# Performance work log

Hardware: AMD Instinct MI355X
Metric: run time of the kernel (lower is better)

## Reference

```python
import jax, jax.numpy as jnp
import numpy as np

EPS = 1e-5

def batchnorm1d(x, g, b):
    # train-mode batch stats over (B, N); x: (B, C, N)
    m = x.mean(axis=(0, 2), keepdims=True)
    v = x.var(axis=(0, 2), keepdims=True)
    return (x - m) * jax.lax.rsqrt(v + EPS) * g[None, :, None] + b[None, :, None]

def instancenorm2d(x, g, b):
    # x: (B, Q, S, K), normalize per-sample per-channel over (S, K)
    m = x.mean(axis=(2, 3), keepdims=True)
    v = x.var(axis=(2, 3), keepdims=True)
    return (x - m) * jax.lax.rsqrt(v + EPS) * g[None, :, None, None] + b[None, :, None, None]

def gather_nbrs(t, idx):
    # t: (B, C, N), idx: (B, S, K) -> (B, C, S, K)
    return jnp.take_along_axis(t[:, :, :, None], idx[:, None, :, :], axis=2)

def pw_conv(x, w, b):
    # 1x1 Conv1d: x (B,C,N), w (O,C), b (O,)
    return jnp.einsum('oc,bcn->bon', w, x) + b[None, :, None]

def fkaconv(x, pos, sup, idx, fc1_w, fc2_w, fc3_w, in1_g, in1_b, in2_g, in2_b,
            alpha, beta, norm_radius, cv_w):
    pts = gather_nbrs(pos, idx) - sup[:, :, :, None]            # (B,3,S,K) local coords
    feat = gather_nbrs(x, idx)                                  # (B,C,S,K)
    # distances computed on detached pts (as in torch)
    d = jnp.sqrt((jax.lax.stop_gradient(pts) ** 2).sum(axis=1))  # (B,S,K)
    dw = jax.nn.sigmoid(-alpha * d + beta)                       # (B,S,K)
    s = dw.sum(axis=2, keepdims=True)
    s = s + (s == 0).astype(dw.dtype) + 1e-6
    dw = (dw / s * d.shape[2])[:, None]                          # (B,1,S,K)
    p = pts / norm_radius
    mat = jax.nn.relu(instancenorm2d(jnp.einsum('qd,bdsk->bqsk', fc1_w, p), in1_g, in1_b))
    mp = jnp.broadcast_to((mat * dw).max(axis=3, keepdims=True), mat.shape)
    mat = jnp.concatenate([mat, mp], axis=1)
    mat = jax.nn.relu(instancenorm2d(jnp.einsum('qc,bcsk->bqsk', fc2_w, mat), in2_g, in2_b))
    mp = jnp.broadcast_to((mat * dw).max(axis=3, keepdims=True), mat.shape)
    mat = jnp.concatenate([mat, mp], axis=1)
    mat = jax.nn.relu(jnp.einsum('qc,bcsk->bqsk', fc3_w, mat)) * dw  # (B,Q,S,K)
    agg = jnp.einsum('bcsk,bqsk->bcsq', feat, mat)               # (B,C,S,Q)
    return jnp.einsum('bcsq,ocq->bos', agg, cv_w)                # (B,O,S)

def setup_inputs() -> dict:
    key = jax.random.key(0)
    ks = iter(jax.random.split(key, 40))
    B, Cin, Cmid, Cout, N, S, K, Q = 16, 128, 64, 256, 8192, 2048, 16, 16
    f = lambda *sh: jax.random.normal(next(ks), sh, dtype=jnp.float32) * 0.05
    inp = {
        'x': jax.random.normal(next(ks), (B, Cin, N), dtype=jnp.float32),
        'pos': jax.random.normal(next(ks), (B, 3, N), dtype=jnp.float32),
        'support_points': jax.random.normal(next(ks), (B, 3, S), dtype=jnp.float32),
        'neighbors_indices': jax.random.randint(next(ks), (B, S, K), 0, N),
        'mask_indices': jnp.ones((B, S, K), dtype=jnp.int32),
        # cv0 + bn0
        'cv0_w': f(Cmid, Cin), 'cv0_b': f(Cmid),
        'bn0_g': jnp.ones((Cmid,), jnp.float32), 'bn0_b': jnp.zeros((Cmid,), jnp.float32),
        # FKAConv params
        'fc1_w': f(Q, 3), 'fc2_w': f(Q, 2 * Q), 'fc3_w': f(Q, 2 * Q),
        'in1_g': jnp.ones((Q,), jnp.float32), 'in1_b': jnp.zeros((Q,), jnp.float32),
        'in2_g': jnp.ones((Q,), jnp.float32), 'in2_b': jnp.zeros((Q,), jnp.float32),
        'alpha': jnp.ones((1,), jnp.float32), 'beta': jnp.ones((1,), jnp.float32),
        'norm_radius': jnp.ones((1,), jnp.float32),
        'cv_w': f(Cmid, Cmid, Q),
        'bn1_g': jnp.ones((Cmid,), jnp.float32), 'bn1_b': jnp.zeros((Cmid,), jnp.float32),
        # cv2 + bn2
        'cv2_w': f(Cout, Cmid), 'cv2_b': f(Cout),
        'bn2_g': jnp.ones((Cout,), jnp.float32), 'bn2_b': jnp.zeros((Cout,), jnp.float32),
        # shortcut
        'sc_w': f(Cout, Cin), 'sc_b': f(Cout),
        'bnsc_g': jnp.ones((Cout,), jnp.float32), 'bnsc_b': jnp.zeros((Cout,), jnp.float32),
    }
    return inp

def reference(x, pos, support_points, neighbors_indices, mask_indices,
              cv0_w, cv0_b, bn0_g, bn0_b,
              fc1_w, fc2_w, fc3_w, in1_g, in1_b, in2_g, in2_b,
              alpha, beta, norm_radius, cv_w, bn1_g, bn1_b,
              cv2_w, cv2_b, bn2_g, bn2_b, sc_w, sc_b, bnsc_g, bnsc_b):
    # sampling() / radius_nn() are passthroughs when precomputed (POCO usage)
    idx = neighbors_indices
    h = jax.nn.relu(batchnorm1d(pw_conv(x, cv0_w, cv0_b), bn0_g, bn0_b))          # (B,64,N)
    h = fkaconv(h, pos, support_points, idx, fc1_w, fc2_w, fc3_w,
                in1_g, in1_b, in2_g, in2_b, alpha, beta, norm_radius, cv_w)       # (B,64,S)
    h = jax.nn.relu(batchnorm1d(h, bn1_g, bn1_b))
    h = batchnorm1d(pw_conv(h, cv2_w, cv2_b), bn2_g, bn2_b)                        # (B,256,S)
    sc = batchnorm1d(pw_conv(x, sc_w, sc_b), bnsc_g, bnsc_b)                       # (B,256,N)
    sc = gather_nbrs(sc, idx).max(axis=3)                                          # max_pool -> (B,256,S)
    return jax.nn.relu(h + sc)

if __name__ == '__main__':
    out = reference(**setup_inputs())
    print(out.shape)
```

## Files before the change

### kernel.cpp

```cpp
#include <hip/hip_runtime.h>
#include <hip/hip_bf16.h>

#define DEV static __device__ __forceinline__

typedef __attribute__((ext_vector_type(8))) short bf16x8;
typedef __attribute__((ext_vector_type(4))) float f32x4;

#define ST_SC_BN0  0
#define ST_SH_BN0  64
#define ST_SC_SC   128
#define ST_SH_SC   384
#define ST_SC_IN1  640
#define ST_SH_IN1  896
#define ST_SC_IN2  1152
#define ST_SH_IN2  1408
#define ST_SC_BN1  1664
#define ST_SH_BN1  1728
#define ST_SC_BN2  1792
#define ST_SH_BN2  2048

DEV float rsum16(float v){
#pragma unroll
  for (int off = 8; off >= 1; off >>= 1) v += __shfl_xor(v, off, 16);
  return v;
}
DEV float rmax16(float v){
#pragma unroll
  for (int off = 8; off >= 1; off >>= 1) v = fmaxf(v, __shfl_xor(v, off, 16));
  return v;
}

__global__ __launch_bounds__(256) void k_prep_w(
    const float* __restrict__ cv0w, const float* __restrict__ scw,
    const float* __restrict__ cvw,  const float* __restrict__ cv2w,
    __hip_bfloat16* __restrict__ wb, __hip_bfloat16* __restrict__ cvb,
    __hip_bfloat16* __restrict__ cv2b)
{
  int i = blockIdx.x * 256 + threadIdx.x;
  if (i < 40960){
    float v = (i < 8192) ? cv0w[i] : scw[i - 8192];
    wb[i] = __float2bfloat16(v);
  } else if (i < 106496){
    cvb[i - 40960] = __float2bfloat16(cvw[i - 40960]);
  } else {
    cv2b[i - 106496] = __float2bfloat16(cv2w[i - 106496]);
  }
}

__global__ __launch_bounds__(256) void k_xpose(
    const float* __restrict__ x, __hip_bfloat16* __restrict__ xb)
{
  __shared__ float t[128][65];
  const int tid = threadIdx.x;
  const int b = blockIdx.x >> 7, nt = blockIdx.x & 127;
  const int n0 = nt << 6;
#pragma unroll
  for (int p = 0; p < 8; p++){
    int row = (p << 4) + (tid >> 4);
    float4 v = *(const float4*)&x[(((size_t)b * 128 + row) << 13) + n0 + ((tid & 15) << 2)];
    t[row][(tid & 15) * 4 + 0] = v.x;
    t[row][(tid & 15) * 4 + 1] = v.y;
    t[row][(tid & 15) * 4 + 2] = v.z;
    t[row][(tid & 15) * 4 + 3] = v.w;
  }
  __syncthreads();
  const int k8 = tid & 15;
#pragma unroll
  for (int p = 0; p < 4; p++){
    int n = (p << 4) + (tid >> 4);
    union { uint4 u; __hip_bfloat16 e[8]; } pk;
#pragma unroll
    for (int j = 0; j < 8; j++) pk.e[j] = __float2bfloat16(t[k8 * 8 + j][n]);
    *(uint4*)&xb[((size_t)(b << 13) + n0 + n) * 128 + k8 * 8] = pk.u;
  }
}

__global__ __launch_bounds__(256) void k1_mfma(
    const __hip_bfloat16* __restrict__ xb, const __hip_bfloat16* __restrict__ wb,
    const float* __restrict__ cv0b, const float* __restrict__ scb,
    __hip_bfloat16* __restrict__ y0t, __hip_bfloat16* __restrict__ sct,
    float* __restrict__ p1)
{
  const int tid = threadIdx.x;
  const int b = blockIdx.x >> 7, nt = blockIdx.x & 127;
  const int n0 = nt << 6;
  const int wv = tid >> 6, l = tid & 63;
  const int lr = l & 15, lg = l >> 4;
  float* p1row = p1 + (size_t)blockIdx.x * 640;

  f32x4 acc[5][4];
#pragma unroll
  for (int i = 0; i < 5; i++)
#pragma unroll
    for (int j = 0; j < 4; j++) acc[i][j] = (f32x4){0.f, 0.f, 0.f, 0.f};

  const __hip_bfloat16* xrow = xb + ((size_t)(b << 13) + n0 + lr) * 128 + lg * 8;
  const __hip_bfloat16* wrow = wb + (size_t)(wv * 80 + lr) * 128 + lg * 8;

#pragma unroll
  for (int ks = 0; ks < 4; ks++){
    bf16x8 B[4], A[5];
#pragma unroll
    for (int nf = 0; nf < 4; nf++) B[nf] = *(const bf16x8*)(xrow + nf * 2048 + ks * 32);
#pragma unroll
    for (int mf = 0; mf < 5; mf++) A[mf] = *(const bf16x8*)(wrow + mf * 2048 + ks * 32);
#pragma unroll
    for (int mf = 0; mf < 5; mf++)
#pragma unroll
      for (int nf = 0; nf < 4; nf++)
        acc[mf][nf] = __builtin_amdgcn_mfma_f32_16x16x32_bf16(A[mf], B[nf], acc[mf][nf], 0, 0, 0);
  }

#pragma unroll
  for (int mf = 0; mf < 5; mf++){
    const int m0 = wv * 80 + mf * 16 + lg * 4;
    float bv[4];
#pragma unroll
    for (int r = 0; r < 4; r++){
      int m = m0 + r;
      bv[r] = (m < 64) ? cv0b[m] : scb[m - 64];
    }
#pragma unroll
    for (int nf = 0; nf < 4; nf++)
#pragma unroll
      for (int r = 0; r < 4; r++) acc[mf][nf][r] += bv[r];

#pragma unroll
    for (int nf = 0; nf < 4; nf++){
      int n = n0 + nf * 16 + lr;
      union { uint2 u; __hip_bfloat16 e[4]; } pk;
#pragma unroll
      for (int r = 0; r < 4; r++) pk.e[r] = __float2bfloat16(acc[mf][nf][r]);
      if (m0 < 64)
        *(uint2*)&y0t[((size_t)(b << 13) + n) * 64 + m0] = pk.u;
      else
        *(uint2*)&sct[((size_t)(b << 13) + n) * 256 + (m0 - 64)] = pk.u;
    }
#pragma unroll
    for (int r = 0; r < 4; r++){
      float ss = 0.f, qq = 0.f;
#pragma unroll
      for (int nf = 0; nf < 4; nf++){ float v = acc[mf][nf][r]; ss += v; qq += v * v; }
#pragma unroll
      for (int off = 8; off >= 1; off >>= 1){
        ss += __shfl_xor(ss, off, 16);
        qq += __shfl_xor(qq, off, 16);
      }
      if (lr == 0){
        int ch = m0 + r;
        p1row[ch]       = ss;
        p1row[320 + ch] = qq;
      }
    }
  }
}

__global__ __launch_bounds__(256) void k_redP1(
    const float* __restrict__ part, int nrows,
    const float* __restrict__ g0, const float* __restrict__ b0,
    const float* __restrict__ gs, const float* __restrict__ bs,
    float inv_cnt, float* __restrict__ stat)
{
  __shared__ f32x4 sh_s[256], sh_q[256];
  const int tid = threadIdx.x;
  const int ch0 = blockIdx.x << 4;
  const int c4 = (tid & 3) << 2;
  const int stripe = tid >> 2;
  f32x4 s = {0.f,0.f,0.f,0.f}, q = {0.f,0.f,0.f,0.f};
  for (int r = stripe; r < nrows; r += 64){
    const float* row = part + (size_t)r * 640;
    s += *(const f32x4*)&row[ch0 + c4];
    q += *(const f32x4*)&row[320 + ch0 + c4];
  }
  sh_s[tid] = s; sh_q[tid] = q;
  __syncthreads();
  for (int off = 128; off >= 4; off >>= 1){
    if (tid < off){ sh_s[tid] += sh_s[tid + off]; sh_q[tid] += sh_q[tid + off]; }
    __syncthreads();
  }
  if (tid < 4){
    f32x4 S = sh_s[tid], Q = sh_q[tid];
#pragma unroll
    for (int j = 0; j < 4; j++){
      int ch = ch0 + (tid << 2) + j;
      float m  = S[j] * inv_cnt;
      float v  = Q[j] * inv_cnt - m * m;
      if (ch < 64){
        float sc = g0[ch] * rsqrtf(v + 1e-5f);
        stat[ST_SC_BN0 + ch] = sc;
        stat[ST_SH_BN0 + ch] = b0[ch] - m * sc;
      } else {
        int c = ch - 64;
        float sc = gs[c] * rsqrtf(v + 1e-5f);
        stat[ST_SC_SC + c] = sc;
        stat[ST_SH_SC + c] = bs[c] - m * sc;
      }
    }
  }
}

__global__ __launch_bounds__(256) void k_redA(
    const float* __restrict__ part, int nrows, int rowstride,
    int sum_off, int sq_off,
    const float* __restrict__ g, const float* __restrict__ bb,
    float inv_cnt, int gmod,
    float* __restrict__ scale, float* __restrict__ shift)
{
  __shared__ f32x4 sh_s[256], sh_q[256];
  const int tid = threadIdx.x;
  const int ch0 = blockIdx.x << 4;
  const int c4 = (tid & 3) << 2;
  const int stripe = tid >> 2;
  f32x4 s = {0.f,0.f,0.f,0.f}, q = {0.f,0.f,0.f,0.f};
  for (int r = stripe; r < nrows; r += 64){
    const float* row = part + (size_t)r * rowstride;
    s += *(const f32x4*)&row[sum_off + ch0 + c4];
    q += *(const f32x4*)&row[sq_off + ch0 + c4];
  }
  sh_s[tid] = s; sh_q[tid] = q;
  __syncthreads();
  for (int off = 128; off >= 4; off >>= 1){
    if (tid < off){ sh_s[tid] += sh_s[tid + off]; sh_q[tid] += sh_q[tid + off]; }
    __syncthreads();
  }
  if (tid < 4){
    f32x4 S = sh_s[tid], Q = sh_q[tid];
#pragma unroll
    for (int j = 0; j < 4; j++){
      int ch = ch0 + (tid << 2) + j;
      float m  = S[j] * inv_cnt;
      float v  = Q[j] * inv_cnt - m * m;
      float sc = g[ch % gmod] * rsqrtf(v + 1e-5f);
      scale[ch] = sc;
      shift[ch] = bb[ch % gmod] - m * sc;
    }
  }
}

__global__ __launch_bounds__(256) void k_redB(
    const float* __restrict__ part, int rows_per_b,
    const float* __restrict__ g, const float* __restrict__ bb, float inv_cnt,
    float* __restrict__ scale, float* __restrict__ shift)
{
  __shared__ f32x4 sh_s[256], sh_q[256];
  const int tid = threadIdx.x;
  const int b = blockIdx.x;
  const int c4 = (tid & 3) << 2;
  const int stripe = tid >> 2;
  const float* base = part + (size_t)b * rows_per_b * 32;
  f32x4 s = {0.f,0.f,0.f,0.f}, q = {0.f,0.f,0.f,0.f};
  for (int r = stripe; r < rows_per_b; r += 64){
    s += *(const f32x4*)&base[r * 32 + c4];
    q += *(const f32x4*)&base[r * 32 + 16 + c4];
  }
  sh_s[tid] = s; sh_q[tid] = q;
  __syncthreads();
  for (int off = 128; off >= 4; off >>= 1){
    if (tid < off){ sh_s[tid] += sh_s[tid + off]; sh_q[tid] += sh_q[tid + off]; }
    __syncthreads();
  }
  if (tid < 4){
    f32x4 S = sh_s[tid], Q = sh_q[tid];
#pragma unroll
    for (int j = 0; j < 4; j++){
      int c = (tid << 2) + j;
      float m  = S[j] * inv_cnt;
      float v  = Q[j] * inv_cnt - m * m;
      float sc = g[c] * rsqrtf(v + 1e-5f);
      scale[b * 16 + c] = sc;
      shift[b * 16 + c] = bb[c] - m * sc;
    }
  }
}

__global__ __launch_bounds__(256) void k_in1_stats(
    const float* __restrict__ pos, const float* __restrict__ sup, const int* __restrict__ nbr,
    const float* __restrict__ fc1, const float* __restrict__ nrp, float* __restrict__ pin1)
{
  const int tid = threadIdx.x;
  const int b  = blockIdx.x >> 7;
  const int st = blockIdx.x & 127;
  const int sl = tid >> 4, k = tid & 15;
  const int s  = (st << 4) + sl;
  const int n  = nbr[((((size_t)b << 11) + s) << 4) + k];
  float* pr = pin1 + ((size_t)blockIdx.x * 4 + (tid >> 6)) * 32;
  const float inr = 1.0f / nrp[0];
  float p0 = (pos[((size_t)b * 3 + 0) * 8192 + n] - sup[((size_t)b * 3 + 0) * 2048 + s]) * inr;
  float p1 = (pos[((size_t)b * 3 + 1) * 8192 + n] - sup[((size_t)b * 3 + 1) * 2048 + s]) * inr;
  float p2 = (pos[((size_t)b * 3 + 2) * 8192 + n] - sup[((size_t)b * 3 + 2) * 2048 + s]) * inr;
#pragma unroll
  for (int q = 0; q < 16; q++){
    float z = fc1[q * 3] * p0 + fc1[q * 3 + 1] * p1 + fc1[q * 3 + 2] * p2;
    float a = z, c = z * z;
#pragma unroll
    for (int off = 32; off >= 1; off >>= 1){
      a += __shfl_xor(a, off, 64);
      c += __shfl_xor(c, off, 64);
    }
    if ((tid & 63) == q){
      pr[q]      = a;
      pr[16 + q] = c;
    }
  }
}

__global__ __launch_bounds__(256) void k_in2_stats(
    const float* __restrict__ pos, const float* __restrict__ sup, const int* __restrict__ nbr,
    const float* __restrict__ fc1, const float* __restrict__ fc2,
    const float* __restrict__ alp, const float* __restrict__ bet, const float* __restrict__ nrp,
    const float* __restrict__ stat, float* __restrict__ pin2)
{
  __shared__ float fc2s[512];
  __shared__ float sc1s[16], sh1s[16];
  const int tid = threadIdx.x;
  const int b  = blockIdx.x >> 7;
  const int st = blockIdx.x & 127;
  fc2s[tid]       = fc2[tid];
  fc2s[tid + 256] = fc2[tid + 256];
  if (tid < 16){
    sc1s[tid] = stat[ST_SC_IN1 + (b << 4) + tid];
    sh1s[tid] = stat[ST_SH_IN1 + (b << 4) + tid];
  }
  __syncthreads();
  const int sl = tid >> 4, k = tid & 15;
  const int s  = (st << 4) + sl;
  const int n  = nbr[((((size_t)b << 11) + s) << 4) + k];
  float* pr = pin2 + ((size_t)blockIdx.x * 4 + (tid >> 6)) * 32;
  float t0 = pos[((size_t)b * 3 + 0) * 8192 + n] - sup[((size_t)b * 3 + 0) * 2048 + s];
  float t1 = pos[((size_t)b * 3 + 1) * 8192 + n] - sup[((size_t)b * 3 + 1) * 2048 + s];
  float t2 = pos[((size_t)b * 3 + 2) * 8192 + n] - sup[((size_t)b * 3 + 2) * 2048 + s];
  float dist = sqrtf(t0 * t0 + t1 * t1 + t2 * t2);
  float dw = 1.0f / (1.0f + expf(alp[0] * dist - bet[0]));
  float ssum = rsum16(dw);
  ssum += (ssum == 0.0f ? 1.0f : 0.0f) + 1e-6f;
  dw = dw / ssum * 16.0f;
  const float inr = 1.0f / nrp[0];
  float p0 = t0 * inr, p1 = t1 * inr, p2 = t2 * inr;
  float m1[16], mp1[16];
#pragma unroll
  for (int q = 0; q < 16; q++){
    float z = fc1[q * 3] * p0 + fc1[q * 3 + 1] * p1 + fc1[q * 3 + 2] * p2;
    m1[q] = fmaxf(z * sc1s[q] + sh1s[q], 0.0f);
  }
#pragma unroll
  for (int q = 0; q < 16; q++) mp1[q] = rmax16(m1[q] * dw);
#pragma unroll
  for (int q = 0; q < 16; q++){
    float z = 0.0f;
#pragma unroll
    for (int j = 0; j < 16; j++) z = fmaf(fc2s[q * 32 + j], m1[j], z);
#pragma unroll
    for (int j = 0; j < 16; j++) z = fmaf(fc2s[q * 32 + 16 + j], mp1[j], z);
    float a = z, c = z * z;
#pragma unroll
    for (int off = 32; off >= 1; off >>= 1){
      a += __shfl_xor(a, off, 64);
      c += __shfl_xor(c, off, 64);
    }
    if ((tid & 63) == q){
      pr[q]      = a;
      pr[16 + q] = c;
    }
  }
}

__global__ __launch_bounds__(256) void k_fka(
    const float* __restrict__ pos, const float* __restrict__ sup, const int* __restrict__ nbr,
    const float* __restrict__ fc1, const float* __restrict__ fc2, const float* __restrict__ fc3,
    const float* __restrict__ alp, const float* __restrict__ bet, const float* __restrict__ nrp,
    const __hip_bfloat16* __restrict__ y0t, const float* __restrict__ stat,
    __hip_bfloat16* __restrict__ agg)
{
  __shared__ float fc2s[512], fc3s[512];
  __shared__ float sc1s[16], sh1s[16], sc2s[16], sh2s[16];
  __shared__ float sc0s[64], sh0s[64];
  __shared__ float mat3_s[16][16][17];
  __shared__ float feat2_s[2][16][65];
  __shared__ int   idx_s[16][16];

  const int tid = threadIdx.x;
  const int b  = blockIdx.x >> 7;
  const int st = blockIdx.x & 127;
  fc2s[tid]       = fc2[tid];
  fc2s[tid + 256] = fc2[tid + 256];
  fc3s[tid]       = fc3[tid];
  fc3s[tid + 256] = fc3[tid + 256];
  if (tid < 16){
    sc1s[tid] = stat[ST_SC_IN1 + (b << 4) + tid];
    sh1s[tid] = stat[ST_SH_IN1 + (b << 4) + tid];
    sc2s[tid] = stat[ST_SC_IN2 + (b << 4) + tid];
    sh2s[tid] = stat[ST_SH_IN2 + (b << 4) + tid];
  }
  if (tid < 64){
    sc0s[tid] = stat[ST_SC_BN0 + tid];
    sh0s[tid] = stat[ST_SH_BN0 + tid];
  }
  const int sl = tid >> 4, k = tid & 15;
  const int s  = (st << 4) + sl;
  const int n  = nbr[((((size_t)b << 11) + s) << 4) + k];
  idx_s[sl][k] = n;
  __syncthreads();

  float t0 = pos[((size_t)b * 3 + 0) * 8192 + n] - sup[((size_t)b * 3 + 0) * 2048 + s];
  float t1 = pos[((size_t)b * 3 + 1) * 8192 + n] - sup[((size_t)b * 3 + 1) * 2048 + s];
  float t2 = pos[((size_t)b * 3 + 2) * 8192 + n] - sup[((size_t)b * 3 + 2) * 2048 + s];
  float dist = sqrtf(t0 * t0 + t1 * t1 + t2 * t2);
  float dw = 1.0f / (1.0f + expf(alp[0] * dist - bet[0]));
  float ssum = rsum16(dw);
  ssum += (ssum == 0.0f ? 1.0f : 0.0f) + 1e-6f;
  dw = dw / ssum * 16.0f;
  const float inr = 1.0f / nrp[0];
  float p0 = t0 * inr, p1 = t1 * inr, p2 = t2 * inr;
  float m1[16], mp1[16];
#pragma unroll
  for (int q = 0; q < 16; q++){
    float z = fc1[q * 3] * p0 + fc1[q * 3 + 1] * p1 + fc1[q * 3 + 2] * p2;
    m1[q] = fmaxf(z * sc1s[q] + sh1s[q], 0.0f);
  }
#pragma unroll
  for (int q = 0; q < 16; q++) mp1[q] = rmax16(m1[q] * dw);
  float m2[16], mp2[16];
#pragma unroll
  for (int q = 0; q < 16; q++){
    float z = 0.0f;
#pragma unroll
    for (int j = 0; j < 16; j++) z = fmaf(fc2s[q * 32 + j], m1[j], z);
#pragma unroll
    for (int j = 0; j < 16; j++) z = fmaf(fc2s[q * 32 + 16 + j], mp1[j], z);
    m2[q] = fmaxf(z * sc2s[q] + sh2s[q], 0.0f);
  }
#pragma unroll
  for (int q = 0; q < 16; q++) mp2[q] = rmax16(m2[q] * dw);
#pragma unroll
  for (int q = 0; q < 16; q++){
    float z = 0.0f;
#pragma unroll
    for (int j = 0; j < 16; j++) z = fmaf(fc3s[q * 32 + j], m2[j], z);
#pragma unroll
    for (int j = 0; j < 16; j++) z = fmaf(fc3s[q * 32 + 16 + j], mp2[j], z);
    mat3_s[sl][q][k] = fmaxf(z, 0.0f) * dw;
  }
  __syncthreads();

  const int h   = tid >> 7;
  const int r7  = tid & 127;
  const int gk  = r7 >> 3;
  const int gc8 = r7 & 7;
  const int cc  = r7 >> 1;
  const int qh  = r7 & 1;

  for (int it = 0; it < 8; it++){
    const int sl2 = it * 2 + h;
    {
      int nn = idx_s[sl2][gk];
      union { uint4 u; __hip_bfloat16 e[8]; } ld;
      ld.u = *(const uint4*)&y0t[((size_t)(b << 13) + nn) * 64 + gc8 * 8];
#pragma unroll
      for (int j = 0; j < 8; j++){
        int ch = gc8 * 8 + j;
        feat2_s[h][gk][ch] = fmaxf(__bfloat162float(ld.e[j]) * sc0s[ch] + sh0s[ch], 0.0f);
      }
    }
    __syncthreads();
    {
      float fv[16];
#pragma unroll
      for (int kk = 0; kk < 16; kk++) fv[kk] = feat2_s[h][kk][cc];
      union { uint4 u; __hip_bfloat16 e[8]; } pk;
#pragma unroll
      for (int q2 = 0; q2 < 8; q2++){
        int q = qh * 8 + q2;
        float a2 = 0.0f;
#pragma unroll
        for (int kk = 0; kk < 16; kk++) a2 = fmaf(fv[kk], mat3_s[sl2][q][kk], a2);
        pk.e[q2] = __float2bfloat16(a2);
      }
      int ss = (st << 4) + sl2;
      *(uint4*)&agg[((size_t)(b << 11) + ss) * 1024 + cc * 16 + qh * 8] = pk.u;
    }
    __syncthreads();
  }
}

__global__ __launch_bounds__(256) void k6_mfma(
    const __hip_bfloat16* __restrict__ agg, const __hip_bfloat16* __restrict__ cvb,
    float* __restrict__ hfka, float* __restrict__ p6)
{
  const int tid = threadIdx.x;
  const int b = blockIdx.x >> 5, stile = blockIdx.x & 31;
  const int wv = tid >> 6, l = tid & 63;
  const int lr = l & 15, lg = l >> 4;
  const int sw = (stile << 6) + (wv << 4);
  float* p6row = p6 + ((size_t)blockIdx.x * 4 + wv) * 128;

  f32x4 acc[4];
#pragma unroll
  for (int i = 0; i < 4; i++) acc[i] = (f32x4){0.f, 0.f, 0.f, 0.f};

  const __hip_bfloat16* brow = agg + ((size_t)(b << 11) + sw + lr) * 1024 + lg * 8;
  const __hip_bfloat16* arow = cvb + (size_t)lr * 1024 + lg * 8;

#pragma unroll 4
  for (int ks = 0; ks < 32; ks++){
    bf16x8 B = *(const bf16x8*)(brow + ks * 32);
    bf16x8 A[4];
#pragma unroll
    for (int mf = 0; mf < 4; mf++) A[mf] = *(const bf16x8*)(arow + mf * 16384 + ks * 32);
#pragma unroll
    for (int mf = 0; mf < 4; mf++)
      acc[mf] = __builtin_amdgcn_mfma_f32_16x16x32_bf16(A[mf], B, acc[mf], 0, 0, 0);
  }

  const int s = sw + lr;
#pragma unroll
  for (int mf = 0; mf < 4; mf++){
    const int m0 = mf * 16 + lg * 4;
    float4 v = make_float4(acc[mf][0], acc[mf][1], acc[mf][2], acc[mf][3]);
    *(float4*)&hfka[((size_t)(b << 11) + s) * 64 + m0] = v;
#pragma unroll
    for (int r = 0; r < 4; r++){
      float ss = acc[mf][r], qq = ss * ss;
#pragma unroll
      for (int off = 8; off >= 1; off >>= 1){
        ss += __shfl_xor(ss, off, 16);
        qq += __shfl_xor(qq, off, 16);
      }
      if (lr == 0){
        p6row[m0 + r]      = ss;
        p6row[64 + m0 + r] = qq;
      }
    }
  }
}

__global__ __launch_bounds__(256) void k7_mfma(
    const float* __restrict__ hfka, const __hip_bfloat16* __restrict__ cv2b,
    const float* __restrict__ bias, const float* __restrict__ stat_ro,
    __hip_bfloat16* __restrict__ h2, float* __restrict__ p7)
{
  const int tid = threadIdx.x;
  const int b = blockIdx.x >> 5, stile = blockIdx.x & 31;
  const int s0 = stile << 6;
  const int wv = tid >> 6, l = tid & 63;
  const int lr = l & 15, lg = l >> 4;
  float* p7row = p7 + (size_t)blockIdx.x * 512;

  float s1r[2][8], h1r[2][8];
#pragma unroll
  for (int ks = 0; ks < 2; ks++)
#pragma unroll
    for (int j = 0; j < 8; j++){
      int ch = ks * 32 + lg * 8 + j;
      s1r[ks][j] = stat_ro[ST_SC_BN1 + ch];
      h1r[ks][j] = stat_ro[ST_SH_BN1 + ch];
    }

  bf16x8 B[2][4];
#pragma unroll
  for (int ks = 0; ks < 2; ks++)
#pragma unroll
    for (int nf = 0; nf < 4; nf++){
      int s = s0 + nf * 16 + lr;
      const float* hp = hfka + ((size_t)(b << 11) + s) * 64 + ks * 32 + lg * 8;
      float4 v0 = *(const float4*)hp;
      float4 v1 = *(const float4*)(hp + 4);
      float vv[8] = {v0.x, v0.y, v0.z, v0.w, v1.x, v1.y, v1.z, v1.w};
      union { bf16x8 f; __hip_bfloat16 e[8]; } pk;
#pragma unroll
      for (int j = 0; j < 8; j++)
        pk.e[j] = __float2bfloat16(fmaxf(vv[j] * s1r[ks][j] + h1r[ks][j], 0.0f));
      B[ks][nf] = pk.f;
    }

  f32x4 acc[4][4];
#pragma unroll
  for (int i = 0; i < 4; i++)
#pragma unroll
    for (int j = 0; j < 4; j++) acc[i][j] = (f32x4){0.f, 0.f, 0.f, 0.f};

  const __hip_bfloat16* arow = cv2b + (size_t)(wv * 64 + lr) * 64 + lg * 8;
#pragma unroll
  for (int ks = 0; ks < 2; ks++){
    bf16x8 A[4];
#pragma unroll
    for (int mf = 0; mf < 4; mf++) A[mf] = *(const bf16x8*)(arow + mf * 1024 + ks * 32);
#pragma unroll
    for (int mf = 0; mf < 4; mf++)
#pragma unroll
      for (int nf = 0; nf < 4; nf++)
        acc[mf][nf] = __builtin_amdgcn_mfma_f32_16x16x32_bf16(A[mf], B[ks][nf], acc[mf][nf], 0, 0, 0);
  }

#pragma unroll
  for (int mf = 0; mf < 4; mf++){
    const int m0 = wv * 64 + mf * 16 + lg * 4;
    float bv[4];
#pragma unroll
    for (int r = 0; r < 4; r++) bv[r] = bias[m0 + r];
#pragma unroll
    for (int nf = 0; nf < 4; nf++){
      int s = s0 + nf * 16 + lr;
      union { uint2 u; __hip_bfloat16 e[4]; } pk;
#pragma unroll
      for (int r = 0; r < 4; r++){
        acc[mf][nf][r] += bv[r];
        pk.e[r] = __float2bfloat16(acc[mf][nf][r]);
      }
      *(uint2*)&h2[((size_t)(b << 11) + s) * 256 + m0] = pk.u;
    }
#pragma unroll
    for (int r = 0; r < 4; r++){
      float ss = 0.f, qq = 0.f;
#pragma unroll
      for (int nf = 0; nf < 4; nf++){ float v = acc[mf][nf][r]; ss += v; qq += v * v; }
#pragma unroll
      for (int off = 8; off >= 1; off >>= 1){
        ss += __shfl_xor(ss, off, 16);
        qq += __shfl_xor(qq, off, 16);
      }
      if (lr == 0){
        p7row[m0 + r]       = ss;
        p7row[256 + m0 + r] = qq;
      }
    }
  }
}

__global__ __launch_bounds__(256) void k_final(
    const __hip_bfloat16* __restrict__ sct, const __hip_bfloat16* __restrict__ h2,
    const int* __restrict__ nbr, const float* __restrict__ stat, float* __restrict__ out)
{
  __shared__ int   idx_s[256];
  __shared__ float tile_s[16][257];
  const int tid = threadIdx.x;
  const int b  = blockIdx.x >> 7;
  const int st = blockIdx.x & 127;
  const int s0 = st << 4;
  idx_s[tid] = nbr[((size_t)(b << 11) + s0) * 16 + tid];
  const int sl = tid >> 4, cg = tid & 15, ch0 = cg << 4;

  float ssc[16], hsc[16], s2v[16], h2v[16];
#pragma unroll
  for (int j = 0; j < 16; j++){
    ssc[j] = stat[ST_SC_SC  + ch0 + j];
    hsc[j] = stat[ST_SH_SC  + ch0 + j];
    s2v[j] = stat[ST_SC_BN2 + ch0 + j];
    h2v[j] = stat[ST_SH_BN2 + ch0 + j];
  }
  __syncthreads();

  float mx[16];
#pragma unroll
  for (int j = 0; j < 16; j++) mx[j] = -3.4e38f;
  for (int k = 0; k < 16; k++){
    int nn = idx_s[sl * 16 + k];
    const uint4* p = (const uint4*)&sct[((size_t)(b << 13) + nn) * 256 + ch0];
    union { uint4 u; __hip_bfloat16 e[8]; } a0, a1;
    a0.u = p[0]; a1.u = p[1];
#pragma unroll
    for (int j = 0; j < 8; j++){
      mx[j]     = fmaxf(mx[j],     __bfloat162float(a0.e[j]) * ssc[j]     + hsc[j]);
      mx[j + 8] = fmaxf(mx[j + 8], __bfloat162float(a1.e[j]) * ssc[j + 8] + hsc[j + 8]);
    }
  }
  {
    const uint4* p = (const uint4*)&h2[((size_t)(b << 11) + s0 + sl) * 256 + ch0];
    union { uint4 u; __hip_bfloat16 e[8]; } a0, a1;
    a0.u = p[0]; a1.u = p[1];
#pragma unroll
    for (int j = 0; j < 8; j++){
      tile_s[sl][ch0 + j]     = fmaxf(__bfloat162float(a0.e[j]) * s2v[j]     + h2v[j]     + mx[j], 0.0f);
      tile_s[sl][ch0 + 8 + j] = fmaxf(__bfloat162float(a1.e[j]) * s2v[j + 8] + h2v[j + 8] + mx[j + 8], 0.0f);
    }
  }
  __syncthreads();
  const int o = tid;
#pragma unroll
  for (int p4 = 0; p4 < 4; p4++){
    float4 v = make_float4(tile_s[p4 * 4 + 0][o], tile_s[p4 * 4 + 1][o],
                           tile_s[p4 * 4 + 2][o], tile_s[p4 * 4 + 3][o]);
    *(float4*)&out[((size_t)(b << 8) + o) * 2048 + s0 + p4 * 4] = v;
  }
}

extern "C" void kernel_launch(void* const* d_in, const int* in_sizes, int n_in,
                              void* d_out, int out_size, void* d_ws, size_t ws_size,
                              hipStream_t stream)
{
  (void)in_sizes; (void)n_in; (void)out_size; (void)ws_size;
  const float* x     = (const float*)d_in[0];
  const float* pos   = (const float*)d_in[1];
  const float* sup   = (const float*)d_in[2];
  const int*   nbr   = (const int*)d_in[3];
  const float* cv0w  = (const float*)d_in[5];
  const float* cv0b  = (const float*)d_in[6];
  const float* bn0g  = (const float*)d_in[7];
  const float* bn0b  = (const float*)d_in[8];
  const float* fc1   = (const float*)d_in[9];
  const float* fc2   = (const float*)d_in[10];
  const float* fc3   = (const float*)d_in[11];
  const float* in1g  = (const float*)d_in[12];
  const float* in1b  = (const float*)d_in[13];
  const float* in2g  = (const float*)d_in[14];
  const float* in2b  = (const float*)d_in[15];
  const float* alp   = (const float*)d_in[16];
  const float* bet   = (const float*)d_in[17];
  const float* nrp   = (const float*)d_in[18];
  const float* cvw   = (const float*)d_in[19];
  const float* bn1g  = (const float*)d_in[20];
  const float* bn1b  = (const float*)d_in[21];
  const float* cv2w  = (const float*)d_in[22];
  const float* cv2bi = (const float*)d_in[23];
  const float* bn2g  = (const float*)d_in[24];
  const float* bn2b  = (const float*)d_in[25];
  const float* scw   = (const float*)d_in[26];
  const float* scb   = (const float*)d_in[27];
  const float* bnscg = (const float*)d_in[28];
  const float* bnscb = (const float*)d_in[29];

  char* w = (char*)d_ws;
  __hip_bfloat16* sct  = (__hip_bfloat16*)(w);
  __hip_bfloat16* y0t  = (__hip_bfloat16*)(w + 67108864);
  __hip_bfloat16* aggp = (__hip_bfloat16*)(w + 83886080);
  __hip_bfloat16* xb   = (__hip_bfloat16*)(w + 83886080);
  float*          pin1 = (float*)(w + 83886080);
  float*          pin2 = (float*)(w + 84934656);
  float*          p7   = (float*)(w + 83886080);
  float*          hfka = (float*)(w + 150994944);
  float*          p1   = (float*)(w + 150994944);
  __hip_bfloat16* h2   = (__hip_bfloat16*)(w + 159383552);
  float*          p6   = (float*)(w + 159383552);
  __hip_bfloat16* wb   = (__hip_bfloat16*)(w + 176160768);
  __hip_bfloat16* cvb  = (__hip_bfloat16*)(w + 176242688);
  __hip_bfloat16* cv2b = (__hip_bfloat16*)(w + 176373760);
  float*          stat = (float*)(w + 192937984UL);

  k_prep_w<<<480, 256, 0, stream>>>(cv0w, scw, cvw, cv2w, wb, cvb, cv2b);
  k_xpose<<<2048, 256, 0, stream>>>(x, xb);
  k1_mfma<<<2048, 256, 0, stream>>>(xb, wb, cv0b, scb, y0t, sct, p1);
  k_redP1<<<20, 256, 0, stream>>>(p1, 2048, bn0g, bn0b, bnscg, bnscb,
                                  1.0f / 131072.0f, stat);
  k_in1_stats<<<2048, 256, 0, stream>>>(pos, sup, nbr, fc1, nrp, pin1);
  k_redB<<<16, 256, 0, stream>>>(pin1, 512, in1g, in1b, 1.0f / 32768.0f,
                                 stat + ST_SC_IN1, stat + ST_SH_IN1);
  k_in2_stats<<<2048, 256, 0, stream>>>(pos, sup, nbr, fc1, fc2, alp, bet, nrp, stat, pin2);
  k_redB<<<16, 256, 0, stream>>>(pin2, 512, in2g, in2b, 1.0f / 32768.0f,
                                 stat + ST_SC_IN2, stat + ST_SH_IN2);
  k_fka<<<2048, 256, 0, stream>>>(pos, sup, nbr, fc1, fc2, fc3, alp, bet, nrp, y0t, stat, aggp);
  k6_mfma<<<512, 256, 0, stream>>>(aggp, cvb, hfka, p6);
  k_redA<<<4, 256, 0, stream>>>(p6, 2048, 128, 0, 64, bn1g, bn1b,
                                1.0f / 32768.0f, 64, stat + ST_SC_BN1, stat + ST_SH_BN1);
  k7_mfma<<<512, 256, 0, stream>>>(hfka, cv2b, cv2bi, stat, h2, p7);
  k_redA<<<16, 256, 0, stream>>>(p7, 512, 512, 0, 256, bn2g, bn2b,
                                 1.0f / 32768.0f, 256, stat + ST_SC_BN2, stat + ST_SH_BN2);
  k_final<<<2048, 256, 0, stream>>>(sct, h2, nbr, stat, (float*)d_out);
}
```

Before: 508.5 us.

## Fuse input transpose into first GEMM and cv GEMM into FKA kernel

```diff
diff --git a/kernel.cpp b/kernel.cpp
--- a/kernel.cpp
+++ b/kernel.cpp
@@ -47,40 +47,13 @@
   }
 }
 
-__global__ __launch_bounds__(256) void k_xpose(
-    const float* __restrict__ x, __hip_bfloat16* __restrict__ xb)
-{
-  __shared__ float t[128][65];
-  const int tid = threadIdx.x;
-  const int b = blockIdx.x >> 7, nt = blockIdx.x & 127;
-  const int n0 = nt << 6;
-#pragma unroll
-  for (int p = 0; p < 8; p++){
-    int row = (p << 4) + (tid >> 4);
-    float4 v = *(const float4*)&x[(((size_t)b * 128 + row) << 13) + n0 + ((tid & 15) << 2)];
-    t[row][(tid & 15) * 4 + 0] = v.x;
-    t[row][(tid & 15) * 4 + 1] = v.y;
-    t[row][(tid & 15) * 4 + 2] = v.z;
-    t[row][(tid & 15) * 4 + 3] = v.w;
-  }
-  __syncthreads();
-  const int k8 = tid & 15;
-#pragma unroll
-  for (int p = 0; p < 4; p++){
-    int n = (p << 4) + (tid >> 4);
-    union { uint4 u; __hip_bfloat16 e[8]; } pk;
-#pragma unroll
-    for (int j = 0; j < 8; j++) pk.e[j] = __float2bfloat16(t[k8 * 8 + j][n]);
-    *(uint4*)&xb[((size_t)(b << 13) + n0 + n) * 128 + k8 * 8] = pk.u;
-  }
-}
-
 __global__ __launch_bounds__(256) void k1_mfma(
-    const __hip_bfloat16* __restrict__ xb, const __hip_bfloat16* __restrict__ wb,
+    const float* __restrict__ x, const __hip_bfloat16* __restrict__ wb,
     const float* __restrict__ cv0b, const float* __restrict__ scb,
     __hip_bfloat16* __restrict__ y0t, __hip_bfloat16* __restrict__ sct,
     float* __restrict__ p1)
 {
+  __shared__ __hip_bfloat16 xt[64][136];
   const int tid = threadIdx.x;
   const int b = blockIdx.x >> 7, nt = blockIdx.x & 127;
   const int n0 = nt << 6;
@@ -88,20 +61,32 @@
   const int lr = l & 15, lg = l >> 4;
   float* p1row = p1 + (size_t)blockIdx.x * 640;
 
+#pragma unroll
+  for (int p = 0; p < 8; p++){
+    int c  = (p << 4) + (tid >> 4);
+    int n4 = (tid & 15) << 2;
+    float4 v = *(const float4*)&x[(((size_t)b * 128 + c) << 13) + n0 + n4];
+    xt[n4 + 0][c] = __float2bfloat16(v.x);
+    xt[n4 + 1][c] = __float2bfloat16(v.y);
+    xt[n4 + 2][c] = __float2bfloat16(v.z);
+    xt[n4 + 3][c] = __float2bfloat16(v.w);
+  }
+  __syncthreads();
+
   f32x4 acc[5][4];
 #pragma unroll
   for (int i = 0; i < 5; i++)
 #pragma unroll
     for (int j = 0; j < 4; j++) acc[i][j] = (f32x4){0.f, 0.f, 0.f, 0.f};
 
-  const __hip_bfloat16* xrow = xb + ((size_t)(b << 13) + n0 + lr) * 128 + lg * 8;
   const __hip_bfloat16* wrow = wb + (size_t)(wv * 80 + lr) * 128 + lg * 8;
 
 #pragma unroll
   for (int ks = 0; ks < 4; ks++){
     bf16x8 B[4], A[5];
 #pragma unroll
-    for (int nf = 0; nf < 4; nf++) B[nf] = *(const bf16x8*)(xrow + nf * 2048 + ks * 32);
+    for (int nf = 0; nf < 4; nf++)
+      B[nf] = *(const bf16x8*)&xt[nf * 16 + lr][ks * 32 + lg * 8];
 #pragma unroll
     for (int mf = 0; mf < 5; mf++) A[mf] = *(const bf16x8*)(wrow + mf * 2048 + ks * 32);
 #pragma unroll
@@ -369,7 +354,8 @@
     const float* __restrict__ fc1, const float* __restrict__ fc2, const float* __restrict__ fc3,
     const float* __restrict__ alp, const float* __restrict__ bet, const float* __restrict__ nrp,
     const __hip_bfloat16* __restrict__ y0t, const float* __restrict__ stat,
-    __hip_bfloat16* __restrict__ agg)
+    __hip_bfloat16* __restrict__ agg, const __hip_bfloat16* __restrict__ cvb,
+    float* __restrict__ hfka, float* __restrict__ p6)
 {
   __shared__ float fc2s[512], fc3s[512];
   __shared__ float sc1s[16], sh1s[16], sc2s[16], sh2s[16];
@@ -480,54 +466,35 @@
     }
     __syncthreads();
   }
-}
-
-__global__ __launch_bounds__(256) void k6_mfma(
-    const __hip_bfloat16* __restrict__ agg, const __hip_bfloat16* __restrict__ cvb,
-    float* __restrict__ hfka, float* __restrict__ p6)
-{
-  const int tid = threadIdx.x;
-  const int b = blockIdx.x >> 5, stile = blockIdx.x & 31;
-  const int wv = tid >> 6, l = tid & 63;
-  const int lr = l & 15, lg = l >> 4;
-  const int sw = (stile << 6) + (wv << 4);
-  float* p6row = p6 + ((size_t)blockIdx.x * 4 + wv) * 128;
-
-  f32x4 acc[4];
-#pragma unroll
-  for (int i = 0; i < 4; i++) acc[i] = (f32x4){0.f, 0.f, 0.f, 0.f};
-
-  const __hip_bfloat16* brow = agg + ((size_t)(b << 11) + sw + lr) * 1024 + lg * 8;
-  const __hip_bfloat16* arow = cvb + (size_t)lr * 1024 + lg * 8;
-
+
+  {
+    const int wv2 = tid >> 6, l2 = tid & 63;
+    const int lr2 = l2 & 15, lg2 = l2 >> 4;
+    const int s0 = st << 4;
+    f32x4 accc = {0.f, 0.f, 0.f, 0.f};
+    const __hip_bfloat16* brow = agg + ((size_t)(b << 11) + s0 + lr2) * 1024 + lg2 * 8;
+    const __hip_bfloat16* arow = cvb + (size_t)(wv2 * 16 + lr2) * 1024 + lg2 * 8;
 #pragma unroll 4
-  for (int ks = 0; ks < 32; ks++){
-    bf16x8 B = *(const bf16x8*)(brow + ks * 32);
-    bf16x8 A[4];
-#pragma unroll
-    for (int mf = 0; mf < 4; mf++) A[mf] = *(const bf16x8*)(arow + mf * 16384 + ks * 32);
-#pragma unroll
-    for (int mf = 0; mf < 4; mf++)
-      acc[mf] = __builtin_amdgcn_mfma_f32_16x16x32_bf16(A[mf], B, acc[mf], 0, 0, 0);
-  }
-
-  const int s = sw + lr;
-#pragma unroll
-  for (int mf = 0; mf < 4; mf++){
-    const int m0 = mf * 16 + lg * 4;
-    float4 v = make_float4(acc[mf][0], acc[mf][1], acc[mf][2], acc[mf][3]);
-    *(float4*)&hfka[((size_t)(b << 11) + s) * 64 + m0] = v;
+    for (int ks = 0; ks < 32; ks++){
+      bf16x8 Bf = *(const bf16x8*)(brow + ks * 32);
+      bf16x8 Af = *(const bf16x8*)(arow + ks * 32);
+      accc = __builtin_amdgcn_mfma_f32_16x16x32_bf16(Af, Bf, accc, 0, 0, 0);
+    }
+    *(float4*)&hfka[((size_t)(b << 11) + s0 + lr2) * 64 + wv2 * 16 + (lg2 << 2)] =
+        make_float4(accc[0], accc[1], accc[2], accc[3]);
+    float* p6row = p6 + (size_t)blockIdx.x * 128;
 #pragma unroll
     for (int r = 0; r < 4; r++){
-      float ss = acc[mf][r], qq = ss * ss;
+      float ss = accc[r], qq = ss * ss;
 #pragma unroll
       for (int off = 8; off >= 1; off >>= 1){
         ss += __shfl_xor(ss, off, 16);
         qq += __shfl_xor(qq, off, 16);
       }
-      if (lr == 0){
-        p6row[m0 + r]      = ss;
-        p6row[64 + m0 + r] = qq;
+      if (lr2 == 0){
+        int ch = wv2 * 16 + (lg2 << 2) + r;
+        p6row[ch]      = ss;
+        p6row[64 + ch] = qq;
       }
     }
   }
@@ -722,7 +689,6 @@
   __hip_bfloat16* sct  = (__hip_bfloat16*)(w);
   __hip_bfloat16* y0t  = (__hip_bfloat16*)(w + 67108864);
   __hip_bfloat16* aggp = (__hip_bfloat16*)(w + 83886080);
-  __hip_bfloat16* xb   = (__hip_bfloat16*)(w + 83886080);
   float*          pin1 = (float*)(w + 83886080);
   float*          pin2 = (float*)(w + 84934656);
   float*          p7   = (float*)(w + 83886080);
@@ -736,8 +702,7 @@
   float*          stat = (float*)(w + 192937984UL);
 
   k_prep_w<<<480, 256, 0, stream>>>(cv0w, scw, cvw, cv2w, wb, cvb, cv2b);
-  k_xpose<<<2048, 256, 0, stream>>>(x, xb);
-  k1_mfma<<<2048, 256, 0, stream>>>(xb, wb, cv0b, scb, y0t, sct, p1);
+  k1_mfma<<<2048, 256, 0, stream>>>(x, wb, cv0b, scb, y0t, sct, p1);
   k_redP1<<<20, 256, 0, stream>>>(p1, 2048, bn0g, bn0b, bnscg, bnscb,
                                   1.0f / 131072.0f, stat);
   k_in1_stats<<<2048, 256, 0, stream>>>(pos, sup, nbr, fc1, nrp, pin1);
@@ -746,8 +711,8 @@
   k_in2_stats<<<2048, 256, 0, stream>>>(pos, sup, nbr, fc1, fc2, alp, bet, nrp, stat, pin2);
   k_redB<<<16, 256, 0, stream>>>(pin2, 512, in2g, in2b, 1.0f / 32768.0f,
                                  stat + ST_SC_IN2, stat + ST_SH_IN2);
-  k_fka<<<2048, 256, 0, stream>>>(pos, sup, nbr, fc1, fc2, fc3, alp, bet, nrp, y0t, stat, aggp);
-  k6_mfma<<<512, 256, 0, stream>>>(aggp, cvb, hfka, p6);
+  k_fka<<<2048, 256, 0, stream>>>(pos, sup, nbr, fc1, fc2, fc3, alp, bet, nrp, y0t, stat,
+                                  aggp, cvb, hfka, p6);
   k_redA<<<4, 256, 0, stream>>>(p6, 2048, 128, 0, 64, bn1g, bn1b,
                                 1.0f / 32768.0f, 64, stat + ST_SC_BN1, stat + ST_SH_BN1);
   k7_mfma<<<512, 256, 0, stream>>>(hfka, cv2b, cv2bi, stat, h2, p7);
```

New measurement: 494.7 us. 1.03x faster.

## Fuse input transpose into k1 and restructure FKA aggregation per thread

Applied to the files above, without the earlier changes.

```diff
diff --git a/kernel.cpp b/kernel.cpp
--- a/kernel.cpp
+++ b/kernel.cpp
@@ -41,46 +41,22 @@
     float v = (i < 8192) ? cv0w[i] : scw[i - 8192];
     wb[i] = __float2bfloat16(v);
   } else if (i < 106496){
-    cvb[i - 40960] = __float2bfloat16(cvw[i - 40960]);
+    int j = i - 40960;
+    int o = j >> 10, kk = j & 1023;
+    int c = kk >> 4, q = kk & 15;
+    cvb[(o << 10) + (q << 6) + c] = __float2bfloat16(cvw[j]);
   } else {
     cv2b[i - 106496] = __float2bfloat16(cv2w[i - 106496]);
   }
 }
 
-__global__ __launch_bounds__(256) void k_xpose(
-    const float* __restrict__ x, __hip_bfloat16* __restrict__ xb)
-{
-  __shared__ float t[128][65];
-  const int tid = threadIdx.x;
-  const int b = blockIdx.x >> 7, nt = blockIdx.x & 127;
-  const int n0 = nt << 6;
-#pragma unroll
-  for (int p = 0; p < 8; p++){
-    int row = (p << 4) + (tid >> 4);
-    float4 v = *(const float4*)&x[(((size_t)b * 128 + row) << 13) + n0 + ((tid & 15) << 2)];
-    t[row][(tid & 15) * 4 + 0] = v.x;
-    t[row][(tid & 15) * 4 + 1] = v.y;
-    t[row][(tid & 15) * 4 + 2] = v.z;
-    t[row][(tid & 15) * 4 + 3] = v.w;
-  }
-  __syncthreads();
-  const int k8 = tid & 15;
-#pragma unroll
-  for (int p = 0; p < 4; p++){
-    int n = (p << 4) + (tid >> 4);
-    union { uint4 u; __hip_bfloat16 e[8]; } pk;
-#pragma unroll
-    for (int j = 0; j < 8; j++) pk.e[j] = __float2bfloat16(t[k8 * 8 + j][n]);
-    *(uint4*)&xb[((size_t)(b << 13) + n0 + n) * 128 + k8 * 8] = pk.u;
-  }
-}
-
 __global__ __launch_bounds__(256) void k1_mfma(
-    const __hip_bfloat16* __restrict__ xb, const __hip_bfloat16* __restrict__ wb,
+    const float* __restrict__ x, const __hip_bfloat16* __restrict__ wb,
     const float* __restrict__ cv0b, const float* __restrict__ scb,
     __hip_bfloat16* __restrict__ y0t, __hip_bfloat16* __restrict__ sct,
     float* __restrict__ p1)
 {
+  __shared__ __hip_bfloat16 xt[64][136];
   const int tid = threadIdx.x;
   const int b = blockIdx.x >> 7, nt = blockIdx.x & 127;
   const int n0 = nt << 6;
@@ -88,20 +64,32 @@
   const int lr = l & 15, lg = l >> 4;
   float* p1row = p1 + (size_t)blockIdx.x * 640;
 
+#pragma unroll
+  for (int p = 0; p < 8; p++){
+    int c  = (p << 4) + (tid >> 4);
+    int n4 = (tid & 15) << 2;
+    float4 v = *(const float4*)&x[(((size_t)b * 128 + c) << 13) + n0 + n4];
+    xt[n4 + 0][c] = __float2bfloat16(v.x);
+    xt[n4 + 1][c] = __float2bfloat16(v.y);
+    xt[n4 + 2][c] = __float2bfloat16(v.z);
+    xt[n4 + 3][c] = __float2bfloat16(v.w);
+  }
+  __syncthreads();
+
   f32x4 acc[5][4];
 #pragma unroll
   for (int i = 0; i < 5; i++)
 #pragma unroll
     for (int j = 0; j < 4; j++) acc[i][j] = (f32x4){0.f, 0.f, 0.f, 0.f};
 
-  const __hip_bfloat16* xrow = xb + ((size_t)(b << 13) + n0 + lr) * 128 + lg * 8;
   const __hip_bfloat16* wrow = wb + (size_t)(wv * 80 + lr) * 128 + lg * 8;
 
 #pragma unroll
   for (int ks = 0; ks < 4; ks++){
     bf16x8 B[4], A[5];
 #pragma unroll
-    for (int nf = 0; nf < 4; nf++) B[nf] = *(const bf16x8*)(xrow + nf * 2048 + ks * 32);
+    for (int nf = 0; nf < 4; nf++)
+      B[nf] = *(const bf16x8*)&xt[nf * 16 + lr][ks * 32 + lg * 8];
 #pragma unroll
     for (int mf = 0; mf < 5; mf++) A[mf] = *(const bf16x8*)(wrow + mf * 2048 + ks * 32);
 #pragma unroll
@@ -374,8 +362,7 @@
   __shared__ float fc2s[512], fc3s[512];
   __shared__ float sc1s[16], sh1s[16], sc2s[16], sh2s[16];
   __shared__ float sc0s[64], sh0s[64];
-  __shared__ float mat3_s[16][16][17];
-  __shared__ float feat2_s[2][16][65];
+  __shared__ float mat3_s[16][17][20];
   __shared__ int   idx_s[16][16];
 
   const int tid = threadIdx.x;
@@ -442,43 +429,43 @@
   }
   __syncthreads();
 
-  const int h   = tid >> 7;
-  const int r7  = tid & 127;
-  const int gk  = r7 >> 3;
-  const int gc8 = r7 & 7;
-  const int cc  = r7 >> 1;
-  const int qh  = r7 & 1;
-
-  for (int it = 0; it < 8; it++){
-    const int sl2 = it * 2 + h;
-    {
-      int nn = idx_s[sl2][gk];
-      union { uint4 u; __hip_bfloat16 e[8]; } ld;
-      ld.u = *(const uint4*)&y0t[((size_t)(b << 13) + nn) * 64 + gc8 * 8];
-#pragma unroll
-      for (int j = 0; j < 8; j++){
-        int ch = gc8 * 8 + j;
-        feat2_s[h][gk][ch] = fmaxf(__bfloat162float(ld.e[j]) * sc0s[ch] + sh0s[ch], 0.0f);
-      }
-    }
-    __syncthreads();
-    {
-      float fv[16];
-#pragma unroll
-      for (int kk = 0; kk < 16; kk++) fv[kk] = feat2_s[h][kk][cc];
-      union { uint4 u; __hip_bfloat16 e[8]; } pk;
-#pragma unroll
-      for (int q2 = 0; q2 < 8; q2++){
-        int q = qh * 8 + q2;
-        float a2 = 0.0f;
-#pragma unroll
-        for (int kk = 0; kk < 16; kk++) a2 = fmaf(fv[kk], mat3_s[sl2][q][kk], a2);
-        pk.e[q2] = __float2bfloat16(a2);
-      }
-      int ss = (st << 4) + sl2;
-      *(uint4*)&agg[((size_t)(b << 11) + ss) * 1024 + cc * 16 + qh * 8] = pk.u;
-    }
-    __syncthreads();
+  const int sB = tid >> 4;
+  const int c4 = (tid & 15) << 2;
+  const float s0a = sc0s[c4],     s0b = sc0s[c4 + 1],
+              s0c = sc0s[c4 + 2], s0d = sc0s[c4 + 3];
+  const float h0a = sh0s[c4],     h0b = sh0s[c4 + 1],
+              h0c = sh0s[c4 + 2], h0d = sh0s[c4 + 3];
+
+  float f0[16], f1[16], f2[16], f3[16];
+#pragma unroll
+  for (int kk = 0; kk < 16; kk++){
+    int nn = idx_s[sB][kk];
+    union { uint2 u; __hip_bfloat16 e[4]; } ld;
+    ld.u = *(const uint2*)&y0t[((size_t)(b << 13) + nn) * 64 + c4];
+    f0[kk] = fmaxf(__bfloat162float(ld.e[0]) * s0a + h0a, 0.0f);
+    f1[kk] = fmaxf(__bfloat162float(ld.e[1]) * s0b + h0b, 0.0f);
+    f2[kk] = fmaxf(__bfloat162float(ld.e[2]) * s0c + h0c, 0.0f);
+    f3[kk] = fmaxf(__bfloat162float(ld.e[3]) * s0d + h0d, 0.0f);
+  }
+
+  __hip_bfloat16* arow = agg + ((size_t)(b << 11) + (st << 4) + sB) * 1024 + c4;
+#pragma unroll
+  for (int q = 0; q < 16; q++){
+    float a0 = 0.f, a1 = 0.f, a2 = 0.f, a3 = 0.f;
+#pragma unroll
+    for (int kk = 0; kk < 16; kk++){
+      float mv = mat3_s[sB][q][kk];
+      a0 = fmaf(f0[kk], mv, a0);
+      a1 = fmaf(f1[kk], mv, a1);
+      a2 = fmaf(f2[kk], mv, a2);
+      a3 = fmaf(f3[kk], mv, a3);
+    }
+    union { uint2 u; __hip_bfloat16 e[4]; } pk;
+    pk.e[0] = __float2bfloat16(a0);
+    pk.e[1] = __float2bfloat16(a1);
+    pk.e[2] = __float2bfloat16(a2);
+    pk.e[3] = __float2bfloat16(a3);
+    *(uint2*)(arow + (q << 6)) = pk.u;
   }
 }
 
@@ -721,23 +708,21 @@
   char* w = (char*)d_ws;
   __hip_bfloat16* sct  = (__hip_bfloat16*)(w);
   __hip_bfloat16* y0t  = (__hip_bfloat16*)(w + 67108864);
-  __hip_bfloat16* aggp = (__hip_bfloat16*)(w + 83886080);
-  __hip_bfloat16* xb   = (__hip_bfloat16*)(w + 83886080);
   float*          pin1 = (float*)(w + 83886080);
   float*          pin2 = (float*)(w + 84934656);
-  float*          p7   = (float*)(w + 83886080);
+  float*          p7   = (float*)(w + 85983232);
+  __hip_bfloat16* aggp = (__hip_bfloat16*)(w + 83886080);
+  __hip_bfloat16* h2   = (__hip_bfloat16*)(w + 100663296);
   float*          hfka = (float*)(w + 150994944);
-  float*          p1   = (float*)(w + 150994944);
-  __hip_bfloat16* h2   = (__hip_bfloat16*)(w + 159383552);
-  float*          p6   = (float*)(w + 159383552);
+  float*          p1   = (float*)(w + 160432128);
+  float*          p6   = (float*)(w + 167772160);
   __hip_bfloat16* wb   = (__hip_bfloat16*)(w + 176160768);
   __hip_bfloat16* cvb  = (__hip_bfloat16*)(w + 176242688);
   __hip_bfloat16* cv2b = (__hip_bfloat16*)(w + 176373760);
   float*          stat = (float*)(w + 192937984UL);
 
   k_prep_w<<<480, 256, 0, stream>>>(cv0w, scw, cvw, cv2w, wb, cvb, cv2b);
-  k_xpose<<<2048, 256, 0, stream>>>(x, xb);
-  k1_mfma<<<2048, 256, 0, stream>>>(xb, wb, cv0b, scb, y0t, sct, p1);
+  k1_mfma<<<2048, 256, 0, stream>>>(x, wb, cv0b, scb, y0t, sct, p1);
   k_redP1<<<20, 256, 0, stream>>>(p1, 2048, bn0g, bn0b, bnscg, bnscb,
                                   1.0f / 131072.0f, stat);
   k_in1_stats<<<2048, 256, 0, stream>>>(pos, sup, nbr, fc1, nrp, pin1);
```

After: 449.3 us. 1.13x faster.
